# Performance work log

Hardware: AMD Instinct MI355X
Metric: run time of the kernel (lower is better)

Reference implementation:

```python
import jax, jax.numpy as jnp
import numpy as np


def setup_inputs() -> dict:
    key = jax.random.key(0)
    k1, k2 = jax.random.split(key)
    x = jax.random.normal(k1, (131072, 256), dtype=jnp.float32)
    centroids = jax.random.normal(k2, (2048, 256), dtype=jnp.float32)
    return {"x": x, "centroids": centroids}


def reference(x, centroids):
    """One k-means step: L2 nearest-centroid assignment + scatter-mean update.

    x:         (n, d) sample vectors
    centroids: (K, d) current centroids
    returns:   (K, d) new centroids
    """
    K = centroids.shape[0]
    # Squared L2 distance argmin; ||x||^2 term is constant per row, drop it.
    # scores[n, K] = ||c_k||^2 - 2 * x_n . c_k
    c_sq = jnp.sum(centroids * centroids, axis=-1)          # (K,)
    scores = c_sq[None, :] - 2.0 * jnp.einsum("nd,kd->nk", x, centroids)
    assigns = jnp.argmin(scores, axis=-1)                    # (n,) int
    # Segment mean update; keep old centroid for empty clusters.
    sums = jax.ops.segment_sum(x, assigns, num_segments=K)   # (K, d)
    counts = jax.ops.segment_sum(jnp.ones((x.shape[0],), x.dtype), assigns,
                                 num_segments=K)             # (K,)
    nonempty = counts > 0
    means = sums / jnp.maximum(counts, 1.0)[:, None]
    new_centroids = jnp.where(nonempty[:, None], means, centroids)
    return new_centroids
```

## Files before the change

kernel.cpp:

```cpp
#include <hip/hip_runtime.h>

typedef unsigned short u16;
typedef unsigned int u32;
typedef __attribute__((ext_vector_type(4)))  int  i32x4;
typedef __attribute__((ext_vector_type(16))) int  i32x16;
typedef __attribute__((ext_vector_type(16))) char i8x16;

#define NPTS 131072
#define DIM  256
#define KC   2048

constexpr float S1  = 0.0625f;
constexpr float S2  = S1 / 254.0f;
constexpr float S3  = S2 * S2 / S1;
constexpr float IS1 = 16.0f;
constexpr float IS2 = 4064.0f;
constexpr float IS3 = 1.0f / S3;
constexpr float W_A = S1 * S1;
constexpr float R2  = 1.0f / 254.0f;
constexpr float R3  = 1.0f / 64516.0f;

__device__ inline void quant3(float v, char& q1, char& q2, char& q3) {
    float a = fminf(fmaxf(rintf(v * IS1), -127.f), 127.f);
    float r1 = fmaf(-a, S1, v);
    float b = fminf(fmaxf(rintf(r1 * IS2), -127.f), 127.f);
    float r2 = fmaf(-b, S2, r1);
    float c = fminf(fmaxf(rintf(r2 * IS3), -127.f), 127.f);
    q1 = (char)a; q2 = (char)b; q3 = (char)c;
}

#define GLD16(gsrc, ldst) \
    __builtin_amdgcn_global_load_lds( \
        (const __attribute__((address_space(1))) void*)(gsrc), \
        (__attribute__((address_space(3))) void*)(ldst), 16, 0, 0)

__global__ void cprep_kernel(const float* __restrict__ cen,
                             char* __restrict__ c_q,
                             float* __restrict__ c_sq,
                             int* __restrict__ hist) {
    if (blockIdx.x < 8) hist[blockIdx.x * 256 + threadIdx.x] = 0;
    const int lane = threadIdx.x & 63;
    const int wv   = threadIdx.x >> 6;
    const int n    = blockIdx.x * 4 + wv;
    float4 v = ((const float4*)(cen + (size_t)n * DIM))[lane];
    float ss = v.x * v.x + v.y * v.y + v.z * v.z + v.w * v.w;
    float fv[4] = {v.x, v.y, v.z, v.w};
    char q1[4], q2[4], q3[4];
#pragma unroll
    for (int j = 0; j < 4; ++j) quant3(fv[j], q1[j], q2[j], q3[j]);
    const int g = n >> 5, r32 = n & 31;
    const int s = lane >> 2;
    const size_t base = ((size_t)((g * 16 + s) * 32 + r32)) * 16 + (lane & 3) * 4;
    u32 p1 = (u32)(unsigned char)q1[0] | ((u32)(unsigned char)q1[1] << 8) |
             ((u32)(unsigned char)q1[2] << 16) | ((u32)(unsigned char)q1[3] << 24);
    u32 p2 = (u32)(unsigned char)q2[0] | ((u32)(unsigned char)q2[1] << 8) |
             ((u32)(unsigned char)q2[2] << 16) | ((u32)(unsigned char)q2[3] << 24);
    u32 p3 = (u32)(unsigned char)q3[0] | ((u32)(unsigned char)q3[1] << 8) |
             ((u32)(unsigned char)q3[2] << 16) | ((u32)(unsigned char)q3[3] << 24);
    *(u32*)(c_q + base) = p1;
    *(u32*)(c_q + (size_t)KC * DIM + base) = p2;
    *(u32*)(c_q + (size_t)2 * KC * DIM + base) = p3;
#pragma unroll
    for (int off = 32; off > 0; off >>= 1) ss += __shfl_xor(ss, off);
    if (lane == 0) c_sq[n] = 0.5f * ss / W_A;
}

__global__ __launch_bounds__(256, 3) void assign_kernel(
    const float* __restrict__ x, const char* __restrict__ c_q,
    const float* __restrict__ c_sq, int* __restrict__ assigns,
    int* __restrict__ hist) {
    __shared__ char lds_c[2 * 24576];

    const int tid  = threadIdx.x;
    const int lane = tid & 63;
    const int wv   = tid >> 6;
    const int l31  = lane & 31;
    const int kh   = lane >> 5;

    const int m = blockIdx.x * 128 + wv * 32 + l31;
    const float4* xr = (const float4*)(x + (size_t)m * DIM);
    i8x16 xq1[8], xq2[8], xq3[8];
#pragma unroll
    for (int kt = 0; kt < 8; ++kt) {
        float tmp[16];
#pragma unroll
        for (int j = 0; j < 4; ++j) {
            float4 f = xr[kt * 8 + kh * 4 + j];
            tmp[j * 4 + 0] = f.x; tmp[j * 4 + 1] = f.y;
            tmp[j * 4 + 2] = f.z; tmp[j * 4 + 3] = f.w;
        }
        i8x16 v1, v2, v3;
#pragma unroll
        for (int j = 0; j < 16; ++j) {
            char a, b, c;
            quant3(tmp[j], a, b, c);
            v1[j] = a; v2[j] = b; v3[j] = c;
        }
        xq1[kt] = v1; xq2[kt] = v2; xq3[kt] = v3;
    }

    const float4* csq4 = (const float4*)c_sq;
    float best = 3.4e38f;
    int bidx = 0;

    const char* cl2 = c_q + (size_t)KC * DIM;
    const char* cl3 = c_q + (size_t)2 * KC * DIM;
    {
        GLD16(c_q + tid * 16,         lds_c + tid * 16);
        GLD16(c_q + (tid + 256) * 16, lds_c + (tid + 256) * 16);
        GLD16(cl2 + tid * 16,         lds_c + 8192 + tid * 16);
        GLD16(cl2 + (tid + 256) * 16, lds_c + 8192 + (tid + 256) * 16);
        GLD16(cl3 + tid * 16,         lds_c + 16384 + tid * 16);
        GLD16(cl3 + (tid + 256) * 16, lds_c + 16384 + (tid + 256) * 16);
    }

    for (int nt = 0; nt < 64; ++nt) {
        const int b = nt & 1;
        __syncthreads();
        if (nt < 63) {
            const size_t so = (size_t)(nt + 1) * 8192;
            char* d = lds_c + (b ^ 1) * 24576;
            GLD16(c_q + so + tid * 16,         d + tid * 16);
            GLD16(c_q + so + (tid + 256) * 16, d + (tid + 256) * 16);
            GLD16(cl2 + so + tid * 16,         d + 8192 + tid * 16);
            GLD16(cl2 + so + (tid + 256) * 16, d + 8192 + (tid + 256) * 16);
            GLD16(cl3 + so + tid * 16,         d + 16384 + tid * 16);
            GLD16(cl3 + so + (tid + 256) * 16, d + 16384 + (tid + 256) * 16);
        }

        i32x16 accA = {}, accB = {}, accC = {};
        const char* cb = lds_c + b * 24576;
#pragma unroll
        for (int kt = 0; kt < 8; ++kt) {
            const int off = ((kt * 2 + kh) * 32 + l31) * 16;
            i32x4 c1 = __builtin_bit_cast(i32x4, *(const i8x16*)(cb + off));
            i32x4 c2 = __builtin_bit_cast(i32x4, *(const i8x16*)(cb + 8192 + off));
            i32x4 c3 = __builtin_bit_cast(i32x4, *(const i8x16*)(cb + 16384 + off));
            i32x4 x1 = __builtin_bit_cast(i32x4, xq1[kt]);
            i32x4 x2 = __builtin_bit_cast(i32x4, xq2[kt]);
            i32x4 x3 = __builtin_bit_cast(i32x4, xq3[kt]);
            accA = __builtin_amdgcn_mfma_i32_32x32x32_i8(c1, x1, accA, 0, 0, 0);
            accB = __builtin_amdgcn_mfma_i32_32x32x32_i8(c1, x2, accB, 0, 0, 0);
            accC = __builtin_amdgcn_mfma_i32_32x32x32_i8(c2, x2, accC, 0, 0, 0);
            accB = __builtin_amdgcn_mfma_i32_32x32x32_i8(c2, x1, accB, 0, 0, 0);
            accC = __builtin_amdgcn_mfma_i32_32x32x32_i8(c1, x3, accC, 0, 0, 0);
            accC = __builtin_amdgcn_mfma_i32_32x32x32_i8(c3, x1, accC, 0, 0, 0);
        }

#pragma unroll
        for (int bq = 0; bq < 4; ++bq) {
            float4 cs = csq4[nt * 8 + 2 * bq + kh];
            const int n0 = nt * 32 + 8 * bq + 4 * kh;
            float csa[4] = {cs.x, cs.y, cs.z, cs.w};
#pragma unroll
            for (int r = 0; r < 4; ++r) {
                const int idx = bq * 4 + r;
                float dot = fmaf((float)accB[idx], R2,
                            fmaf((float)accC[idx], R3, (float)accA[idx]));
                float v = csa[r] - dot;
                if (v < best) { best = v; bidx = n0 + r; }
            }
        }
    }

    float oval = __shfl_xor(best, 32);
    int   oidx = __shfl_xor(bidx, 32);
    if (oval < best || (oval == best && oidx < bidx)) { best = oval; bidx = oidx; }
    if (lane < 32) {
        assigns[m] = bidx;
        atomicAdd(&hist[bidx], 1);
    }
}

__global__ void scan_kernel(const int* __restrict__ hist,
                            int* __restrict__ base_,
                            int* __restrict__ cursor) {
    __shared__ int tmp[256];
    const int tid = threadIdx.x;
    int v[8], s = 0;
#pragma unroll
    for (int j = 0; j < 8; ++j) { v[j] = hist[tid * 8 + j]; s += v[j]; }
    tmp[tid] = s;
    __syncthreads();
    for (int off = 1; off < 256; off <<= 1) {
        int t = (tid >= off) ? tmp[tid - off] : 0;
        __syncthreads();
        tmp[tid] += t;
        __syncthreads();
    }
    int ex = tmp[tid] - s;
#pragma unroll
    for (int j = 0; j < 8; ++j) {
        base_[tid * 8 + j] = ex;
        cursor[tid * 8 + j] = ex;
        ex += v[j];
    }
}

__global__ void reorder_kernel(const int* __restrict__ assigns,
                               int* __restrict__ cursor,
                               int* __restrict__ order) {
    const int p = blockIdx.x * 256 + threadIdx.x;
    const int a = assigns[p];
    int pos = atomicAdd(&cursor[a], 1);
    order[pos] = p;
}

__global__ void reduce_kernel(const float* __restrict__ x,
                              const int* __restrict__ order,
                              const int* __restrict__ assigns,
                              float* __restrict__ sums) {
    const int tid = threadIdx.x;
    const int r0 = blockIdx.x * 256;
    float acc = 0.f;
    int cur = assigns[order[r0]];
    for (int r = 0; r < 256; r += 4) {
        int p0 = order[r0 + r + 0], p1 = order[r0 + r + 1];
        int p2 = order[r0 + r + 2], p3 = order[r0 + r + 3];
        float v0 = x[(size_t)p0 * DIM + tid];
        float v1 = x[(size_t)p1 * DIM + tid];
        float v2 = x[(size_t)p2 * DIM + tid];
        float v3 = x[(size_t)p3 * DIM + tid];
        int a0 = assigns[p0], a1 = assigns[p1], a2 = assigns[p2], a3 = assigns[p3];
        if (a0 != cur) { unsafeAtomicAdd(&sums[(size_t)cur * DIM + tid], acc); acc = 0.f; cur = a0; }
        acc += v0;
        if (a1 != cur) { unsafeAtomicAdd(&sums[(size_t)cur * DIM + tid], acc); acc = 0.f; cur = a1; }
        acc += v1;
        if (a2 != cur) { unsafeAtomicAdd(&sums[(size_t)cur * DIM + tid], acc); acc = 0.f; cur = a2; }
        acc += v2;
        if (a3 != cur) { unsafeAtomicAdd(&sums[(size_t)cur * DIM + tid], acc); acc = 0.f; cur = a3; }
        acc += v3;
    }
    unsafeAtomicAdd(&sums[(size_t)cur * DIM + tid], acc);
}

__global__ void finalize_kernel(const float* __restrict__ sums,
                                const int* __restrict__ hist,
                                const float* __restrict__ cen,
                                float* __restrict__ out) {
    const int id = blockIdx.x * 256 + threadIdx.x;
    const int k = id >> 6;
    const int cnt = hist[k];
    float4 s = ((const float4*)sums)[id];
    float4 c = ((const float4*)cen)[id];
    float4 o;
    if (cnt > 0) {
        float r = 1.0f / (float)cnt;
        o.x = s.x * r; o.y = s.y * r; o.z = s.z * r; o.w = s.w * r;
    } else {
        o = c;
    }
    ((float4*)out)[id] = o;
}

extern "C" void kernel_launch(void* const* d_in, const int* in_sizes, int n_in,
                              void* d_out, int out_size, void* d_ws, size_t ws_size,
                              hipStream_t stream) {
    (void)in_sizes; (void)n_in; (void)out_size; (void)ws_size;
    const float* x   = (const float*)d_in[0];
    const float* cen = (const float*)d_in[1];
    float* out = (float*)d_out;

    char* ws = (char*)d_ws;
    size_t off = 0;
    char* c_q = (char*)(ws + off);           off += (size_t)3 * KC * DIM;
    float* c_sq = (float*)(ws + off);        off += (size_t)KC * 4;
    int* assigns = (int*)(ws + off);         off += (size_t)NPTS * 4;
    int* hist = (int*)(ws + off);            off += (size_t)KC * 4;
    int* base_ = (int*)(ws + off);           off += (size_t)KC * 4;
    int* cursor = (int*)(ws + off);          off += (size_t)KC * 4;
    int* order = (int*)(ws + off);           off += (size_t)NPTS * 4;
    float* sums = (float*)(ws + off);        off += (size_t)KC * DIM * 4;

    hipMemsetAsync(sums, 0, (size_t)KC * DIM * sizeof(float), stream);
    cprep_kernel<<<KC / 4, 256, 0, stream>>>(cen, c_q, c_sq, hist);
    assign_kernel<<<NPTS / 128, 256, 0, stream>>>(x, c_q, c_sq, assigns, hist);
    scan_kernel<<<1, 256, 0, stream>>>(hist, base_, cursor);
    reorder_kernel<<<NPTS / 256, 256, 0, stream>>>(assigns, cursor, order);
    reduce_kernel<<<NPTS / 256, 256, 0, stream>>>(x, order, assigns, sums);
    finalize_kernel<<<KC * 64 / 256, 256, 0, stream>>>(sums, hist, cen, out);
}
```

Measured before the change: 625.2 us.

## Split centroid range across two blocks per point tile, merge via 64-bit atomicMin

Each point tile is now handled by two blocks, each scanning half of the centroids, which doubles the grid size. Per-point results are combined with an atomicMin on a packed (order-preserving float score, index) 64-bit key. A new resolve kernel then writes the assignments and the histogram. The goal is better occupancy and load balance across CUs (1024 blocks to 2048), at the cost of quantising x twice, an extra memset, an extra kernel and global atomics.

```diff
diff --git a/kernel.cpp b/kernel.cpp
--- a/kernel.cpp
+++ b/kernel.cpp
@@ -2,6 +2,7 @@
 
 typedef unsigned short u16;
 typedef unsigned int u32;
+typedef unsigned long long u64;
 typedef __attribute__((ext_vector_type(4)))  int  i32x4;
 typedef __attribute__((ext_vector_type(16))) int  i32x16;
 typedef __attribute__((ext_vector_type(16))) char i8x16;
@@ -9,6 +10,7 @@
 #define NPTS 131072
 #define DIM  256
 #define KC   2048
+#define HALF_NT 32
 
 constexpr float S1  = 0.0625f;
 constexpr float S2  = S1 / 254.0f;
@@ -67,8 +69,7 @@
 
 __global__ __launch_bounds__(256, 3) void assign_kernel(
     const float* __restrict__ x, const char* __restrict__ c_q,
-    const float* __restrict__ c_sq, int* __restrict__ assigns,
-    int* __restrict__ hist) {
+    const float* __restrict__ c_sq, u64* __restrict__ best_key) {
     __shared__ char lds_c[2 * 24576];
 
     const int tid  = threadIdx.x;
@@ -76,8 +77,10 @@
     const int wv   = tid >> 6;
     const int l31  = lane & 31;
     const int kh   = lane >> 5;
-
-    const int m = blockIdx.x * 128 + wv * 32 + l31;
+    const int pc   = blockIdx.x >> 1;
+    const int h    = blockIdx.x & 1;
+
+    const int m = pc * 128 + wv * 32 + l31;
     const float4* xr = (const float4*)(x + (size_t)m * DIM);
     i8x16 xq1[8], xq2[8], xq3[8];
 #pragma unroll
@@ -103,25 +106,27 @@
     float best = 3.4e38f;
     int bidx = 0;
 
-    const char* cl2 = c_q + (size_t)KC * DIM;
-    const char* cl3 = c_q + (size_t)2 * KC * DIM;
+    const size_t ho = (size_t)h * (HALF_NT * 8192);
+    const char* cl1 = c_q + ho;
+    const char* cl2 = c_q + (size_t)KC * DIM + ho;
+    const char* cl3 = c_q + (size_t)2 * KC * DIM + ho;
     {
-        GLD16(c_q + tid * 16,         lds_c + tid * 16);
-        GLD16(c_q + (tid + 256) * 16, lds_c + (tid + 256) * 16);
+        GLD16(cl1 + tid * 16,         lds_c + tid * 16);
+        GLD16(cl1 + (tid + 256) * 16, lds_c + (tid + 256) * 16);
         GLD16(cl2 + tid * 16,         lds_c + 8192 + tid * 16);
         GLD16(cl2 + (tid + 256) * 16, lds_c + 8192 + (tid + 256) * 16);
         GLD16(cl3 + tid * 16,         lds_c + 16384 + tid * 16);
         GLD16(cl3 + (tid + 256) * 16, lds_c + 16384 + (tid + 256) * 16);
     }
 
-    for (int nt = 0; nt < 64; ++nt) {
-        const int b = nt & 1;
+    for (int t = 0; t < HALF_NT; ++t) {
+        const int b = t & 1;
         __syncthreads();
-        if (nt < 63) {
-            const size_t so = (size_t)(nt + 1) * 8192;
+        if (t < HALF_NT - 1) {
+            const size_t so = (size_t)(t + 1) * 8192;
             char* d = lds_c + (b ^ 1) * 24576;
-            GLD16(c_q + so + tid * 16,         d + tid * 16);
-            GLD16(c_q + so + (tid + 256) * 16, d + (tid + 256) * 16);
+            GLD16(cl1 + so + tid * 16,         d + tid * 16);
+            GLD16(cl1 + so + (tid + 256) * 16, d + (tid + 256) * 16);
             GLD16(cl2 + so + tid * 16,         d + 8192 + tid * 16);
             GLD16(cl2 + so + (tid + 256) * 16, d + 8192 + (tid + 256) * 16);
             GLD16(cl3 + so + tid * 16,         d + 16384 + tid * 16);
@@ -147,6 +152,7 @@
             accC = __builtin_amdgcn_mfma_i32_32x32x32_i8(c3, x1, accC, 0, 0, 0);
         }
 
+        const int nt = h * HALF_NT + t;
 #pragma unroll
         for (int bq = 0; bq < 4; ++bq) {
             float4 cs = csq4[nt * 8 + 2 * bq + kh];
@@ -167,9 +173,20 @@
     int   oidx = __shfl_xor(bidx, 32);
     if (oval < best || (oval == best && oidx < bidx)) { best = oval; bidx = oidx; }
     if (lane < 32) {
-        assigns[m] = bidx;
-        atomicAdd(&hist[bidx], 1);
-    }
+        u32 sb = __float_as_uint(best);
+        sb = (sb & 0x80000000u) ? ~sb : (sb | 0x80000000u);
+        u64 key = ((u64)sb << 32) | (u32)bidx;
+        atomicMin(&best_key[m], key);
+    }
+}
+
+__global__ void resolve_kernel(const u64* __restrict__ best_key,
+                               int* __restrict__ assigns,
+                               int* __restrict__ hist) {
+    const int m = blockIdx.x * 256 + threadIdx.x;
+    const int idx = (int)(u32)(best_key[m] & 0xffffffffu);
+    assigns[m] = idx;
+    atomicAdd(&hist[idx], 1);
 }
 
 __global__ void scan_kernel(const int* __restrict__ hist,
@@ -271,10 +288,13 @@
     int* cursor = (int*)(ws + off);          off += (size_t)KC * 4;
     int* order = (int*)(ws + off);           off += (size_t)NPTS * 4;
     float* sums = (float*)(ws + off);        off += (size_t)KC * DIM * 4;
+    u64* best_key = (u64*)(ws + off);        off += (size_t)NPTS * 8;
 
     hipMemsetAsync(sums, 0, (size_t)KC * DIM * sizeof(float), stream);
+    hipMemsetAsync(best_key, 0xFF, (size_t)NPTS * sizeof(u64), stream);
     cprep_kernel<<<KC / 4, 256, 0, stream>>>(cen, c_q, c_sq, hist);
-    assign_kernel<<<NPTS / 128, 256, 0, stream>>>(x, c_q, c_sq, assigns, hist);
+    assign_kernel<<<2 * NPTS / 128, 256, 0, stream>>>(x, c_q, c_sq, best_key);
+    resolve_kernel<<<NPTS / 256, 256, 0, stream>>>(best_key, assigns, hist);
     scan_kernel<<<1, 256, 0, stream>>>(hist, base_, cursor);
     reorder_kernel<<<NPTS / 256, 256, 0, stream>>>(assigns, cursor, order);
     reduce_kernel<<<NPTS / 256, 256, 0, stream>>>(x, order, assigns, sums);
```

New measurement: 678.2 us. 8.5% more time.

## Triple-buffer centroid tiles with explicit vmcnt waits and integer score epilogue

Applied to the files above, without the earlier changes.

Replaces the double-buffered 8 KB-per-plane centroid pipeline with a 3-stage ring of half-size (4 KB-per-plane) stages. Each stage is gated by explicit s_waitcnt vmcnt and a raw s_barrier, and MFMA priority is raised with s_setprio. Centroid squared norms are prescaled to integers and cached in LDS, so the epilogue combines accA and accB in integer arithmetic and does one float fma, instead of three int-to-float conversions from global loads. The clamps on the second and third quantization levels are dropped, which relies on the residuals staying in int8 range, and the scaled-integer rounding of norms slightly changes tie-breaking precision.

```diff
diff --git a/kernel.cpp b/kernel.cpp
--- a/kernel.cpp
+++ b/kernel.cpp
@@ -2,6 +2,7 @@
 
 typedef unsigned short u16;
 typedef unsigned int u32;
+typedef unsigned long long u64;
 typedef __attribute__((ext_vector_type(4)))  int  i32x4;
 typedef __attribute__((ext_vector_type(16))) int  i32x16;
 typedef __attribute__((ext_vector_type(16))) char i8x16;
@@ -18,14 +19,13 @@
 constexpr float IS3 = 1.0f / S3;
 constexpr float W_A = S1 * S1;
 constexpr float R2  = 1.0f / 254.0f;
-constexpr float R3  = 1.0f / 64516.0f;
 
 __device__ inline void quant3(float v, char& q1, char& q2, char& q3) {
     float a = fminf(fmaxf(rintf(v * IS1), -127.f), 127.f);
     float r1 = fmaf(-a, S1, v);
-    float b = fminf(fmaxf(rintf(r1 * IS2), -127.f), 127.f);
+    float b = rintf(r1 * IS2);
     float r2 = fmaf(-b, S2, r1);
-    float c = fminf(fmaxf(rintf(r2 * IS3), -127.f), 127.f);
+    float c = rintf(r2 * IS3);
     q1 = (char)a; q2 = (char)b; q3 = (char)c;
 }
 
@@ -36,7 +36,7 @@
 
 __global__ void cprep_kernel(const float* __restrict__ cen,
                              char* __restrict__ c_q,
-                             float* __restrict__ c_sq,
+                             int* __restrict__ c_sqi,
                              int* __restrict__ hist) {
     if (blockIdx.x < 8) hist[blockIdx.x * 256 + threadIdx.x] = 0;
     const int lane = threadIdx.x & 63;
@@ -62,14 +62,14 @@
     *(u32*)(c_q + (size_t)2 * KC * DIM + base) = p3;
 #pragma unroll
     for (int off = 32; off > 0; off >>= 1) ss += __shfl_xor(ss, off);
-    if (lane == 0) c_sq[n] = 0.5f * ss / W_A;
+    if (lane == 0) c_sqi[n] = (int)rintf(ss * (0.5f * 254.0f / W_A));
 }
 
 __global__ __launch_bounds__(256, 3) void assign_kernel(
     const float* __restrict__ x, const char* __restrict__ c_q,
-    const float* __restrict__ c_sq, int* __restrict__ assigns,
+    const int* __restrict__ c_sqi, int* __restrict__ assigns,
     int* __restrict__ hist) {
-    __shared__ char lds_c[2 * 24576];
+    __shared__ char lds_c[3 * 12288 + 8192];
 
     const int tid  = threadIdx.x;
     const int lane = tid & 63;
@@ -77,6 +77,19 @@
     const int l31  = lane & 31;
     const int kh   = lane >> 5;
 
+    const char* cl1 = c_q;
+    const char* cl2 = c_q + (size_t)KC * DIM;
+    const char* cl3 = c_q + (size_t)2 * KC * DIM;
+
+    GLD16((const char*)c_sqi + tid * 16,         lds_c + 36864 + tid * 16);
+    GLD16((const char*)c_sqi + (tid + 256) * 16, lds_c + 36864 + (tid + 256) * 16);
+    GLD16(cl1 + tid * 16,        lds_c + tid * 16);
+    GLD16(cl2 + tid * 16,        lds_c + 4096 + tid * 16);
+    GLD16(cl3 + tid * 16,        lds_c + 8192 + tid * 16);
+    GLD16(cl1 + 4096 + tid * 16, lds_c + 12288 + tid * 16);
+    GLD16(cl2 + 4096 + tid * 16, lds_c + 12288 + 4096 + tid * 16);
+    GLD16(cl3 + 4096 + tid * 16, lds_c + 12288 + 8192 + tid * 16);
+
     const int m = blockIdx.x * 128 + wv * 32 + l31;
     const float4* xr = (const float4*)(x + (size_t)m * DIM);
     i8x16 xq1[8], xq2[8], xq3[8];
@@ -99,65 +112,66 @@
         xq1[kt] = v1; xq2[kt] = v2; xq3[kt] = v3;
     }
 
-    const float4* csq4 = (const float4*)c_sq;
+    __syncthreads();
+
     float best = 3.4e38f;
     int bidx = 0;
-
-    const char* cl2 = c_q + (size_t)KC * DIM;
-    const char* cl3 = c_q + (size_t)2 * KC * DIM;
-    {
-        GLD16(c_q + tid * 16,         lds_c + tid * 16);
-        GLD16(c_q + (tid + 256) * 16, lds_c + (tid + 256) * 16);
-        GLD16(cl2 + tid * 16,         lds_c + 8192 + tid * 16);
-        GLD16(cl2 + (tid + 256) * 16, lds_c + 8192 + (tid + 256) * 16);
-        GLD16(cl3 + tid * 16,         lds_c + 16384 + tid * 16);
-        GLD16(cl3 + (tid + 256) * 16, lds_c + 16384 + (tid + 256) * 16);
-    }
-
-    for (int nt = 0; nt < 64; ++nt) {
-        const int b = nt & 1;
-        __syncthreads();
-        if (nt < 63) {
-            const size_t so = (size_t)(nt + 1) * 8192;
-            char* d = lds_c + (b ^ 1) * 24576;
-            GLD16(c_q + so + tid * 16,         d + tid * 16);
-            GLD16(c_q + so + (tid + 256) * 16, d + (tid + 256) * 16);
-            GLD16(cl2 + so + tid * 16,         d + 8192 + tid * 16);
-            GLD16(cl2 + so + (tid + 256) * 16, d + 8192 + (tid + 256) * 16);
-            GLD16(cl3 + so + tid * 16,         d + 16384 + tid * 16);
-            GLD16(cl3 + so + (tid + 256) * 16, d + 16384 + (tid + 256) * 16);
-        }
-
+    int b3 = 0;
+
+    const int* csqL = (const int*)(lds_c + 36864);
+
+    for (int t = 0; t < 64; ++t) {
         i32x16 accA = {}, accB = {}, accC = {};
-        const char* cb = lds_c + b * 24576;
-#pragma unroll
-        for (int kt = 0; kt < 8; ++kt) {
-            const int off = ((kt * 2 + kh) * 32 + l31) * 16;
-            i32x4 c1 = __builtin_bit_cast(i32x4, *(const i8x16*)(cb + off));
-            i32x4 c2 = __builtin_bit_cast(i32x4, *(const i8x16*)(cb + 8192 + off));
-            i32x4 c3 = __builtin_bit_cast(i32x4, *(const i8x16*)(cb + 16384 + off));
-            i32x4 x1 = __builtin_bit_cast(i32x4, xq1[kt]);
-            i32x4 x2 = __builtin_bit_cast(i32x4, xq2[kt]);
-            i32x4 x3 = __builtin_bit_cast(i32x4, xq3[kt]);
-            accA = __builtin_amdgcn_mfma_i32_32x32x32_i8(c1, x1, accA, 0, 0, 0);
-            accB = __builtin_amdgcn_mfma_i32_32x32x32_i8(c1, x2, accB, 0, 0, 0);
-            accC = __builtin_amdgcn_mfma_i32_32x32x32_i8(c2, x2, accC, 0, 0, 0);
-            accB = __builtin_amdgcn_mfma_i32_32x32x32_i8(c2, x1, accB, 0, 0, 0);
-            accC = __builtin_amdgcn_mfma_i32_32x32x32_i8(c1, x3, accC, 0, 0, 0);
-            accC = __builtin_amdgcn_mfma_i32_32x32x32_i8(c3, x1, accC, 0, 0, 0);
+#pragma unroll
+        for (int h2 = 0; h2 < 2; ++h2) {
+            if (t == 63 && h2 == 1) {
+                asm volatile("s_waitcnt vmcnt(0)" ::: "memory");
+            } else {
+                asm volatile("s_waitcnt vmcnt(3)" ::: "memory");
+            }
+            __builtin_amdgcn_s_barrier();
+            __builtin_amdgcn_sched_barrier(0);
+            if (2 * t + h2 + 2 < 128) {
+                int pn = b3 + 2; if (pn >= 3) pn -= 3;
+                char* d = lds_c + pn * 12288;
+                const size_t so = (size_t)(2 * t + h2 + 2) * 4096;
+                GLD16(cl1 + so + tid * 16, d + tid * 16);
+                GLD16(cl2 + so + tid * 16, d + 4096 + tid * 16);
+                GLD16(cl3 + so + tid * 16, d + 8192 + tid * 16);
+            }
+            const char* cb = lds_c + b3 * 12288;
+            __builtin_amdgcn_s_setprio(1);
+#pragma unroll
+            for (int kt2 = 0; kt2 < 4; ++kt2) {
+                const int off = kt2 * 1024 + kh * 512 + l31 * 16;
+                i32x4 c1 = __builtin_bit_cast(i32x4, *(const i8x16*)(cb + off));
+                i32x4 c2 = __builtin_bit_cast(i32x4, *(const i8x16*)(cb + 4096 + off));
+                i32x4 c3 = __builtin_bit_cast(i32x4, *(const i8x16*)(cb + 8192 + off));
+                i32x4 x1 = __builtin_bit_cast(i32x4, xq1[h2 * 4 + kt2]);
+                i32x4 x2 = __builtin_bit_cast(i32x4, xq2[h2 * 4 + kt2]);
+                i32x4 x3 = __builtin_bit_cast(i32x4, xq3[h2 * 4 + kt2]);
+                accA = __builtin_amdgcn_mfma_i32_32x32x32_i8(c1, x1, accA, 0, 0, 0);
+                accB = __builtin_amdgcn_mfma_i32_32x32x32_i8(c1, x2, accB, 0, 0, 0);
+                accC = __builtin_amdgcn_mfma_i32_32x32x32_i8(c2, x2, accC, 0, 0, 0);
+                accB = __builtin_amdgcn_mfma_i32_32x32x32_i8(c2, x1, accB, 0, 0, 0);
+                accC = __builtin_amdgcn_mfma_i32_32x32x32_i8(c1, x3, accC, 0, 0, 0);
+                accC = __builtin_amdgcn_mfma_i32_32x32x32_i8(c3, x1, accC, 0, 0, 0);
+            }
+            __builtin_amdgcn_s_setprio(0);
+            b3 += 1; if (b3 == 3) b3 = 0;
         }
 
 #pragma unroll
         for (int bq = 0; bq < 4; ++bq) {
-            float4 cs = csq4[nt * 8 + 2 * bq + kh];
-            const int n0 = nt * 32 + 8 * bq + 4 * kh;
-            float csa[4] = {cs.x, cs.y, cs.z, cs.w};
+            int4 cs = *(const int4*)(csqL + (t * 8 + 2 * bq + kh) * 4);
+            const int n0 = t * 32 + 8 * bq + 4 * kh;
+            int csa[4] = {cs.x, cs.y, cs.z, cs.w};
 #pragma unroll
             for (int r = 0; r < 4; ++r) {
                 const int idx = bq * 4 + r;
-                float dot = fmaf((float)accB[idx], R2,
-                            fmaf((float)accC[idx], R3, (float)accA[idx]));
-                float v = csa[r] - dot;
+                int D  = __mul24(accA[idx], 254) + accB[idx];
+                int Vi = csa[r] - D;
+                float v = fmaf((float)accC[idx], -R2, (float)Vi);
                 if (v < best) { best = v; bidx = n0 + r; }
             }
         }
@@ -264,7 +278,7 @@
     char* ws = (char*)d_ws;
     size_t off = 0;
     char* c_q = (char*)(ws + off);           off += (size_t)3 * KC * DIM;
-    float* c_sq = (float*)(ws + off);        off += (size_t)KC * 4;
+    int* c_sqi = (int*)(ws + off);           off += (size_t)KC * 4;
     int* assigns = (int*)(ws + off);         off += (size_t)NPTS * 4;
     int* hist = (int*)(ws + off);            off += (size_t)KC * 4;
     int* base_ = (int*)(ws + off);           off += (size_t)KC * 4;
@@ -273,8 +287,8 @@
     float* sums = (float*)(ws + off);        off += (size_t)KC * DIM * 4;
 
     hipMemsetAsync(sums, 0, (size_t)KC * DIM * sizeof(float), stream);
-    cprep_kernel<<<KC / 4, 256, 0, stream>>>(cen, c_q, c_sq, hist);
-    assign_kernel<<<NPTS / 128, 256, 0, stream>>>(x, c_q, c_sq, assigns, hist);
+    cprep_kernel<<<KC / 4, 256, 0, stream>>>(cen, c_q, c_sqi, hist);
+    assign_kernel<<<NPTS / 128, 256, 0, stream>>>(x, c_q, c_sqi, assigns, hist);
     scan_kernel<<<1, 256, 0, stream>>>(hist, base_, cursor);
     reorder_kernel<<<NPTS / 256, 256, 0, stream>>>(assigns, cursor, order);
     reduce_kernel<<<NPTS / 256, 256, 0, stream>>>(x, order, assigns, sums);
```

After: 615.3 us. About the same (-1.6%).
